# Optimization experiments

Measured on AMD Instinct MI355X. Metric: run time of the kernel, lower is better.

The kernel has to match this reference:

```python
import jax, jax.numpy as jnp
import numpy as np

B, L, D = 4, 8192, 256          # batch, seq length, embedding dim
H, HD = 8, 32                   # heads, head dim (H*HD == D)
WN, P, S = 9, 4, 1              # window size, padding, stride
EPS = 1e-5


def _layer_norm(x, g, b):
    m = jnp.mean(x, axis=-1, keepdims=True)
    v = jnp.mean(jnp.square(x - m), axis=-1, keepdims=True)
    return (x - m) / jnp.sqrt(v + EPS) * g + b


def setup_inputs() -> dict:
    key = jax.random.key(0)
    ks = jax.random.split(key, 8)
    sc = 0.05
    return {
        "x": jax.random.normal(ks[0], (B, L, D), jnp.float32),
        "W_q": jax.random.normal(ks[1], (D, D), jnp.float32) * sc,
        "W_k": jax.random.normal(ks[2], (D, D), jnp.float32) * sc,
        "W_v": jax.random.normal(ks[3], (D, D), jnp.float32) * sc,
        "W_o": jax.random.normal(ks[4], (D, D), jnp.float32) * sc,
        "pos": jax.random.normal(ks[5], (WN, D), jnp.float32) * sc,
        "W_out": jax.random.normal(ks[6], (D, D), jnp.float32) * sc,
        "b_out": jnp.zeros((D,), jnp.float32),
        "g1": jnp.ones((D,), jnp.float32),
        "b1": jnp.zeros((D,), jnp.float32),
        "g2": jnp.ones((D,), jnp.float32),
        "b2": jnp.zeros((D,), jnp.float32),
    }


def reference(x, W_q, W_k, W_v, W_o, pos, W_out, b_out, g1, b1, g2, b2):
    # input_dim == embedding_dim -> no input projection
    padded = jnp.pad(x, ((0, 0), (P, P), (0, 0)))
    nw = (L + 2 * P - WN) // S + 1  # == L for S=1, WN=2P+1
    idx = jnp.arange(nw)[:, None] * S + jnp.arange(WN)[None, :]  # [nw, WN]
    win = padded[:, idx] + pos  # [B, nw, WN, D]

    def proj(w):  # [B, nw, WN, H, HD]
        return jnp.einsum('bnwd,de->bnwe', win, w).reshape(B, nw, WN, H, HD)

    q, k, v = proj(W_q), proj(W_k), proj(W_v)
    scale = 1.0 / (HD ** 0.5)
    scores = jnp.einsum('bnqhd,bnkhd->bnhqk', q, k) * scale  # [B,nw,H,WN,WN]
    attn = jax.nn.softmax(scores, axis=-1)
    # context, summed over query positions within each window (use_mean=False)
    ctx = jnp.einsum('bnhqk,bnkhd->bnhd', attn, v).reshape(B, nw, D)
    skip = x[:, ::S]  # [B, nw, D]
    attn_res = _layer_norm(skip + ctx @ W_o, g1, b1)
    out = _layer_norm(attn_res @ W_out.T + b_out + attn_res, g2, b2)
    return jax.nn.relu(out)
```

## Files before the change

kernel.cpp:

```cpp
#include <hip/hip_runtime.h>
#include <hip/hip_bf16.h>
#include <math.h>

constexpr int NB   = 4;
constexpr int LL   = 8192;
constexpr int DD   = 256;
constexpr int NH   = 8;
constexpr int HDIM = 32;
constexpr int WNN  = 9;
constexpr int PPAD = 4;

constexpr int CW  = 32;
constexpr int RSN = CW + 8;
constexpr int SST = 260;

typedef __attribute__((ext_vector_type(8))) short bf16x8;
typedef __attribute__((ext_vector_type(4))) float f32x4;

__device__ inline short f2bf(float f) {
  __hip_bfloat16 h = __float2bfloat16(f);
  short s; __builtin_memcpy(&s, &h, 2); return s;
}
__device__ inline float bf2f(short s) {
  unsigned u = ((unsigned)(unsigned short)s) << 16;
  float f; __builtin_memcpy(&f, &u, 4); return f;
}

__global__ __launch_bounds__(256) void prep_all(
    const float* __restrict__ Wq, const float* __restrict__ Wk, const float* __restrict__ Wv,
    const float* __restrict__ Wo, const float* __restrict__ Wout, const float* __restrict__ pos,
    short* __restrict__ WqT, short* __restrict__ WkT, short* __restrict__ WvT,
    short* __restrict__ WoT, short* __restrict__ WoutB,
    short* __restrict__ PQb, short* __restrict__ PKb, short* __restrict__ PVb) {
  __shared__ float sm[64 * 65];
  const int t = threadIdx.x, b = blockIdx.x;
  if (b < 64) {
    const int wi = b >> 4, tile = b & 15;
    const int r0 = (tile >> 2) * 64, c0 = (tile & 3) * 64;
    const float* W = (wi == 0) ? Wq : (wi == 1) ? Wk : (wi == 2) ? Wv : Wo;
    short* T = (wi == 0) ? WqT : (wi == 1) ? WkT : (wi == 2) ? WvT : WoT;
    const int tr = t >> 6, tc = t & 63;
#pragma unroll
    for (int i = 0; i < 16; ++i) {
      int r = tr + i * 4;
      sm[r * 65 + tc] = W[(size_t)(r0 + r) * 256 + c0 + tc];
    }
    __syncthreads();
#pragma unroll
    for (int i = 0; i < 16; ++i) {
      int cj = tr + i * 4;
      T[(size_t)(c0 + cj) * 256 + r0 + tc] = f2bf(sm[tc * 65 + cj]);
    }
  } else if (b < 68) {
    const int idx = b - 64;
    for (int i = t; i < 4096; i += 256) {
      float4 v = *(const float4*)(Wout + ((size_t)idx * 4096 + i) * 4);
      short4 o; o.x = f2bf(v.x); o.y = f2bf(v.y); o.z = f2bf(v.z); o.w = f2bf(v.w);
      *(short4*)(WoutB + ((size_t)idx * 4096 + i) * 4) = o;
    }
  } else {
    const int wh = b - 68;
    const float* W = (wh == 0) ? Wq : (wh == 1) ? Wk : Wv;
    short* P = (wh == 0) ? PQb : (wh == 1) ? PKb : PVb;
    for (int i = t; i < WNN * 256; i += 256) sm[i] = pos[i];
    __syncthreads();
    float a[WNN];
#pragma unroll
    for (int w = 0; w < WNN; ++w) a[w] = 0.f;
    for (int d = 0; d < 256; ++d) {
      float wv = W[(size_t)d * 256 + t];
#pragma unroll
      for (int w = 0; w < WNN; ++w) a[w] += sm[w * 256 + d] * wv;
    }
#pragma unroll
    for (int w = 0; w < WNN; ++w) P[w * 256 + t] = f2bf(a[w]);
  }
}

__global__ __launch_bounds__(256) void qkv_fused(
    const float* __restrict__ x,
    const short* __restrict__ WT0, const short* __restrict__ WT1, const short* __restrict__ WT2,
    short* __restrict__ O0, short* __restrict__ O1, short* __restrict__ O2) {
  __shared__ short xs[32 * 264];
  const int t = threadIdx.x, w = t >> 6, lane = t & 63, q = lane >> 4, m = lane & 15;
  const size_t row0 = (size_t)blockIdx.x * 32;

#pragma unroll
  for (int i = 0; i < 8; ++i) {
    int idx = t + i * 256;
    int r = idx >> 6, c4 = (idx & 63) * 4;
    float4 v = *(const float4*)(x + (row0 + r) * 256 + c4);
    short4 o; o.x = f2bf(v.x); o.y = f2bf(v.y); o.z = f2bf(v.z); o.w = f2bf(v.w);
    *(short4*)&xs[r * 264 + c4] = o;
  }
  __syncthreads();

  f32x4 acc[3][2][4];
#pragma unroll
  for (int bu = 0; bu < 3; ++bu)
#pragma unroll
    for (int i = 0; i < 2; ++i)
#pragma unroll
      for (int j = 0; j < 4; ++j) acc[bu][i][j] = (f32x4){0.f, 0.f, 0.f, 0.f};

#pragma unroll
  for (int kk = 0; kk < 8; ++kk) {
    bf16x8 a[2];
#pragma unroll
    for (int i = 0; i < 2; ++i) a[i] = *(const bf16x8*)&xs[(i * 16 + m) * 264 + kk * 32 + q * 8];
#pragma unroll
    for (int bu = 0; bu < 3; ++bu) {
      const short* WT = (bu == 0) ? WT0 : (bu == 1) ? WT1 : WT2;
#pragma unroll
      for (int j = 0; j < 4; ++j) {
        bf16x8 bb = *(const bf16x8*)(WT + (size_t)(w * 64 + j * 16 + m) * 256 + kk * 32 + q * 8);
#pragma unroll
        for (int i = 0; i < 2; ++i)
          acc[bu][i][j] = __builtin_amdgcn_mfma_f32_16x16x32_bf16(a[i], bb, acc[bu][i][j], 0, 0, 0);
      }
    }
  }
#pragma unroll
  for (int bu = 0; bu < 3; ++bu) {
    short* O = (bu == 0) ? O0 : (bu == 1) ? O1 : O2;
#pragma unroll
    for (int i = 0; i < 2; ++i)
#pragma unroll
      for (int j = 0; j < 4; ++j)
#pragma unroll
        for (int r = 0; r < 4; ++r)
          O[(row0 + i * 16 + q * 4 + r) * 256 + w * 64 + j * 16 + m] = f2bf(acc[bu][i][j][r]);
  }
}

__global__ __launch_bounds__(256, 2) void attn_kernel(
    const short* __restrict__ XQb, const short* __restrict__ XKb, const short* __restrict__ XVb,
    const short* __restrict__ PQb, const short* __restrict__ PKb, const short* __restrict__ PVb,
    short* __restrict__ CTXB) {
  __shared__ short sq[RSN * SST];
  __shared__ short sk[RSN * SST];
  __shared__ short sv[RSN * SST];
  __shared__ short pq[WNN * SST];
  __shared__ short pk[WNN * SST];
  __shared__ short pv[WNN * SST];

  const int t = threadIdx.x;
  const int nblk = LL / CW;
  const int b = blockIdx.x / nblk;
  const int n0 = (blockIdx.x % nblk) * CW;
  const size_t base = (size_t)b * LL * DD;

#pragma unroll
  for (int i = 0; i < RSN * 64 / 256; ++i) {
    int idx = t + i * 256;
    int r = idx >> 6, c4 = (idx & 63) * 4;
    int j = n0 - PPAD + r;
    short4 vq = {0, 0, 0, 0}, vk = vq, vv = vq;
    if (j >= 0 && j < LL) {
      size_t off = base + (size_t)j * DD + c4;
      vq = *(const short4*)(XQb + off);
      vk = *(const short4*)(XKb + off);
      vv = *(const short4*)(XVb + off);
    }
    *(short4*)&sq[r * SST + c4] = vq;
    *(short4*)&sk[r * SST + c4] = vk;
    *(short4*)&sv[r * SST + c4] = vv;
  }
#pragma unroll
  for (int i = 0; i < 3; ++i) {
    int idx = t + i * 256;
    if (idx < WNN * 64) {
      int r = idx >> 6, c4 = (idx & 63) * 4;
      *(short4*)&pq[r * SST + c4] = *(const short4*)(PQb + r * DD + c4);
      *(short4*)&pk[r * SST + c4] = *(const short4*)(PKb + r * DD + c4);
      *(short4*)&pv[r * SST + c4] = *(const short4*)(PVb + r * DD + c4);
    }
  }
  __syncthreads();

  const int n = t >> 3;
  const int h = t & 7;
  const int hoff = h * HDIM;

  float sc[WNN][WNN];
#pragma unroll
  for (int qi = 0; qi < WNN; ++qi)
#pragma unroll
    for (int ki = 0; ki < WNN; ++ki) sc[qi][ki] = 0.f;

#pragma unroll
  for (int c = 0; c < 8; ++c) {
    float qv[WNN][4], kv[WNN][4];
#pragma unroll
    for (int r = 0; r < WNN; ++r) {
      short4 xa = *(const short4*)&sq[(n + r) * SST + hoff + c * 4];
      short4 pa = *(const short4*)&pq[r * SST + hoff + c * 4];
      qv[r][0] = bf2f(xa.x) + bf2f(pa.x);
      qv[r][1] = bf2f(xa.y) + bf2f(pa.y);
      qv[r][2] = bf2f(xa.z) + bf2f(pa.z);
      qv[r][3] = bf2f(xa.w) + bf2f(pa.w);
      short4 xb = *(const short4*)&sk[(n + r) * SST + hoff + c * 4];
      short4 pb = *(const short4*)&pk[r * SST + hoff + c * 4];
      kv[r][0] = bf2f(xb.x) + bf2f(pb.x);
      kv[r][1] = bf2f(xb.y) + bf2f(pb.y);
      kv[r][2] = bf2f(xb.z) + bf2f(pb.z);
      kv[r][3] = bf2f(xb.w) + bf2f(pb.w);
    }
#pragma unroll
    for (int qi = 0; qi < WNN; ++qi)
#pragma unroll
      for (int ki = 0; ki < WNN; ++ki)
        sc[qi][ki] += qv[qi][0] * kv[ki][0] + qv[qi][1] * kv[ki][1] +
                      qv[qi][2] * kv[ki][2] + qv[qi][3] * kv[ki][3];
  }

  float cs[WNN];
#pragma unroll
  for (int ki = 0; ki < WNN; ++ki) cs[ki] = 0.f;
  const float scale = 0.17677669529663687f;
#pragma unroll
  for (int qi = 0; qi < WNN; ++qi) {
    float mx = sc[qi][0];
#pragma unroll
    for (int ki = 1; ki < WNN; ++ki) mx = fmaxf(mx, sc[qi][ki]);
    float sum = 0.f;
    float e[WNN];
#pragma unroll
    for (int ki = 0; ki < WNN; ++ki) { e[ki] = __expf((sc[qi][ki] - mx) * scale); sum += e[ki]; }
    float inv = 1.f / sum;
#pragma unroll
    for (int ki = 0; ki < WNN; ++ki) cs[ki] += e[ki] * inv;
  }

#pragma unroll
  for (int c = 0; c < 8; ++c) {
    float o0 = 0.f, o1 = 0.f, o2 = 0.f, o3 = 0.f;
#pragma unroll
    for (int ki = 0; ki < WNN; ++ki) {
      short4 xv4 = *(const short4*)&sv[(n + ki) * SST + hoff + c * 4];
      short4 pv4 = *(const short4*)&pv[ki * SST + hoff + c * 4];
      float wt = cs[ki];
      o0 += wt * (bf2f(xv4.x) + bf2f(pv4.x));
      o1 += wt * (bf2f(xv4.y) + bf2f(pv4.y));
      o2 += wt * (bf2f(xv4.z) + bf2f(pv4.z));
      o3 += wt * (bf2f(xv4.w) + bf2f(pv4.w));
    }
    short4 os; os.x = f2bf(o0); os.y = f2bf(o1); os.z = f2bf(o2); os.w = f2bf(o3);
    *(short4*)(CTXB + base + (size_t)(n0 + n) * DD + hoff + c * 4) = os;
  }
}

__global__ __launch_bounds__(256) void out_mfma(
    const short* __restrict__ CTXB, const float* __restrict__ X,
    const short* __restrict__ WoT, const short* __restrict__ WoutB,
    const float* __restrict__ bo,
    const float* __restrict__ g1, const float* __restrict__ b1,
    const float* __restrict__ g2, const float* __restrict__ b2,
    float* __restrict__ out) {
  __shared__ short ar[64 * 264];
  __shared__ float ws1[64][4], ws2[64][4];
  __shared__ float msh[64], rsh[64];
  __shared__ float g1s[256], b1s[256], g2s[256], b2s[256], bos[256];
  const int t = threadIdx.x, w = t >> 6, lane = t & 63, q = lane >> 4, m = lane & 15;
  const size_t row0 = (size_t)blockIdx.x * 64;
  g1s[t] = g1[t]; b1s[t] = b1[t]; g2s[t] = g2[t]; b2s[t] = b2[t]; bos[t] = bo[t];

  f32x4 acc[4][4];
#pragma unroll
  for (int i = 0; i < 4; ++i)
#pragma unroll
    for (int j = 0; j < 4; ++j) acc[i][j] = (f32x4){0.f, 0.f, 0.f, 0.f};

  const short* abase = CTXB + (row0 + m) * (size_t)256 + q * 8;
  const short* bbase = WoT + (size_t)(w * 64 + m) * 256 + q * 8;
  {
    bf16x8 a[4], b[4];
#pragma unroll
    for (int i = 0; i < 4; ++i) a[i] = *(const bf16x8*)(abase + (size_t)i * 4096);
#pragma unroll
    for (int j = 0; j < 4; ++j) b[j] = *(const bf16x8*)(bbase + (size_t)j * 4096);
#pragma unroll
    for (int kk = 0; kk < 8; ++kk) {
      bf16x8 an[4], bn[4];
      if (kk < 7) {
#pragma unroll
        for (int i = 0; i < 4; ++i) an[i] = *(const bf16x8*)(abase + (size_t)i * 4096 + (kk + 1) * 32);
#pragma unroll
        for (int j = 0; j < 4; ++j) bn[j] = *(const bf16x8*)(bbase + (size_t)j * 4096 + (kk + 1) * 32);
      }
#pragma unroll
      for (int i = 0; i < 4; ++i)
#pragma unroll
        for (int j = 0; j < 4; ++j)
          acc[i][j] = __builtin_amdgcn_mfma_f32_16x16x32_bf16(a[i], b[j], acc[i][j], 0, 0, 0);
      if (kk < 7) {
#pragma unroll
        for (int i = 0; i < 4; ++i) a[i] = an[i];
#pragma unroll
        for (int j = 0; j < 4; ++j) b[j] = bn[j];
      }
    }
  }

  float s1v[4][4], s2v[4][4];
#pragma unroll
  for (int i = 0; i < 4; ++i)
#pragma unroll
    for (int r = 0; r < 4; ++r) {
      float a0 = 0.f, b0 = 0.f;
#pragma unroll
      for (int j = 0; j < 4; ++j) {
        float v = acc[i][j][r] + X[(row0 + i * 16 + q * 4 + r) * 256 + w * 64 + j * 16 + m];
        acc[i][j][r] = v; a0 += v; b0 += v * v;
      }
      s1v[i][r] = a0; s2v[i][r] = b0;
    }
#pragma unroll
  for (int i = 0; i < 4; ++i)
#pragma unroll
    for (int r = 0; r < 4; ++r)
#pragma unroll
      for (int msk = 1; msk < 16; msk <<= 1) {
        s1v[i][r] += __shfl_xor(s1v[i][r], msk, 64);
        s2v[i][r] += __shfl_xor(s2v[i][r], msk, 64);
      }
  if (m == 0) {
#pragma unroll
    for (int i = 0; i < 4; ++i)
#pragma unroll
      for (int r = 0; r < 4; ++r) {
        ws1[i * 16 + q * 4 + r][w] = s1v[i][r];
        ws2[i * 16 + q * 4 + r][w] = s2v[i][r];
      }
  }
  __syncthreads();
  if (t < 64) {
    float a0 = 0.f, b0 = 0.f;
#pragma unroll
    for (int ww = 0; ww < 4; ++ww) { a0 += ws1[t][ww]; b0 += ws2[t][ww]; }
    float mean = a0 * (1.f / 256.f);
    float var = b0 * (1.f / 256.f) - mean * mean;
    msh[t] = mean; rsh[t] = rsqrtf(var + 1e-5f);
  }
  __syncthreads();

#pragma unroll
  for (int i = 0; i < 4; ++i)
#pragma unroll
    for (int r = 0; r < 4; ++r) {
      int row = i * 16 + q * 4 + r;
      float mean = msh[row], rst = rsh[row];
#pragma unroll
      for (int j = 0; j < 4; ++j) {
        int col = w * 64 + j * 16 + m;
        float v = (acc[i][j][r] - mean) * rst * g1s[col] + b1s[col];
        ar[row * 264 + col] = f2bf(v);
      }
    }
  __syncthreads();

#pragma unroll
  for (int i = 0; i < 4; ++i)
#pragma unroll
    for (int j = 0; j < 4; ++j) acc[i][j] = (f32x4){0.f, 0.f, 0.f, 0.f};
  const short* b2base = WoutB + (size_t)(w * 64 + m) * 256 + q * 8;
  {
    bf16x8 b[4];
#pragma unroll
    for (int j = 0; j < 4; ++j) b[j] = *(const bf16x8*)(b2base + (size_t)j * 4096);
#pragma unroll
    for (int kk = 0; kk < 8; ++kk) {
      bf16x8 bn[4];
      if (kk < 7) {
#pragma unroll
        for (int j = 0; j < 4; ++j) bn[j] = *(const bf16x8*)(b2base + (size_t)j * 4096 + (kk + 1) * 32);
      }
      bf16x8 a[4];
#pragma unroll
      for (int i = 0; i < 4; ++i) a[i] = *(const bf16x8*)&ar[(i * 16 + m) * 264 + kk * 32 + q * 8];
#pragma unroll
      for (int i = 0; i < 4; ++i)
#pragma unroll
        for (int j = 0; j < 4; ++j)
          acc[i][j] = __builtin_amdgcn_mfma_f32_16x16x32_bf16(a[i], b[j], acc[i][j], 0, 0, 0);
      if (kk < 7) {
#pragma unroll
        for (int j = 0; j < 4; ++j) b[j] = bn[j];
      }
    }
  }

#pragma unroll
  for (int i = 0; i < 4; ++i)
#pragma unroll
    for (int r = 0; r < 4; ++r) {
      int row = i * 16 + q * 4 + r;
      float a0 = 0.f, b0 = 0.f;
#pragma unroll
      for (int j = 0; j < 4; ++j) {
        int col = w * 64 + j * 16 + m;
        float v = acc[i][j][r] + bos[col] + bf2f(ar[row * 264 + col]);
        acc[i][j][r] = v; a0 += v; b0 += v * v;
      }
      s1v[i][r] = a0; s2v[i][r] = b0;
    }
#pragma unroll
  for (int i = 0; i < 4; ++i)
#pragma unroll
    for (int r = 0; r < 4; ++r)
#pragma unroll
      for (int msk = 1; msk < 16; msk <<= 1) {
        s1v[i][r] += __shfl_xor(s1v[i][r], msk, 64);
        s2v[i][r] += __shfl_xor(s2v[i][r], msk, 64);
      }
  if (m == 0) {
#pragma unroll
    for (int i = 0; i < 4; ++i)
#pragma unroll
      for (int r = 0; r < 4; ++r) {
        ws1[i * 16 + q * 4 + r][w] = s1v[i][r];
        ws2[i * 16 + q * 4 + r][w] = s2v[i][r];
      }
  }
  __syncthreads();
  if (t < 64) {
    float a0 = 0.f, b0 = 0.f;
#pragma unroll
    for (int ww = 0; ww < 4; ++ww) { a0 += ws1[t][ww]; b0 += ws2[t][ww]; }
    float mean = a0 * (1.f / 256.f);
    float var = b0 * (1.f / 256.f) - mean * mean;
    msh[t] = mean; rsh[t] = rsqrtf(var + 1e-5f);
  }
  __syncthreads();

#pragma unroll
  for (int i = 0; i < 4; ++i)
#pragma unroll
    for (int r = 0; r < 4; ++r) {
      int row = i * 16 + q * 4 + r;
      float mean = msh[row], rst = rsh[row];
#pragma unroll
      for (int j = 0; j < 4; ++j) {
        int col = w * 64 + j * 16 + m;
        float v = (acc[i][j][r] - mean) * rst * g2s[col] + b2s[col];
        out[(row0 + row) * 256 + col] = fmaxf(v, 0.f);
      }
    }
}

extern "C" void kernel_launch(void* const* d_in, const int* in_sizes, int n_in,
                              void* d_out, int out_size, void* d_ws, size_t ws_size,
                              hipStream_t stream) {
  const float* x    = (const float*)d_in[0];
  const float* Wq   = (const float*)d_in[1];
  const float* Wk   = (const float*)d_in[2];
  const float* Wv   = (const float*)d_in[3];
  const float* Wo   = (const float*)d_in[4];
  const float* pos  = (const float*)d_in[5];
  const float* Wout = (const float*)d_in[6];
  const float* bo   = (const float*)d_in[7];
  const float* g1   = (const float*)d_in[8];
  const float* b1   = (const float*)d_in[9];
  const float* g2   = (const float*)d_in[10];
  const float* b2   = (const float*)d_in[11];
  float* out = (float*)d_out;

  const size_t nel = (size_t)NB * LL * DD;
  char* wsb = (char*)d_ws;
  short* XQb  = (short*)wsb; wsb += nel * 2;
  short* XKb  = (short*)wsb; wsb += nel * 2;
  short* XVb  = (short*)wsb; wsb += nel * 2;
  short* CTXB = (short*)wsb; wsb += nel * 2;
  short* WqT   = (short*)wsb; wsb += 65536 * 2;
  short* WkT   = (short*)wsb; wsb += 65536 * 2;
  short* WvT   = (short*)wsb; wsb += 65536 * 2;
  short* WoT   = (short*)wsb; wsb += 65536 * 2;
  short* WoutB = (short*)wsb; wsb += 65536 * 2;
  short* PQb = (short*)wsb; wsb += WNN * DD * 2;
  short* PKb = (short*)wsb; wsb += WNN * DD * 2;
  short* PVb = (short*)wsb; wsb += WNN * DD * 2;

  prep_all<<<71, 256, 0, stream>>>(Wq, Wk, Wv, Wo, Wout, pos,
                                   WqT, WkT, WvT, WoT, WoutB, PQb, PKb, PVb);
  qkv_fused<<<(unsigned)(NB * LL / 32), 256, 0, stream>>>(x, WqT, WkT, WvT, XQb, XKb, XVb);
  attn_kernel<<<NB * (LL / CW), 256, 0, stream>>>(XQb, XKb, XVb, PQb, PKb, PVb, CTXB);
  out_mfma<<<(unsigned)(NB * LL / 64), 256, 0, stream>>>(CTXB, x, WoT, WoutB, bo, g1, b1, g2, b2, out);
}
```

Baseline: 273.1 us.

## Fuse QKV projection, windowed attention and output MLP into one kernel

Replaces the three kernels (QKV GEMM, attention, output GEMMs with layer norms) with a single kernel per 16-row chunk. The QKV projection is recomputed over the chunk plus halo rows and kept in shared memory, the context is written back to shared memory, and the two output GEMMs run on 16 rows. This removes the global round trips of the bf16 Q/K/V and context buffers. In exchange it recomputes halo rows (24 of 32 tile rows are useful), lowers MFMA tile reuse, uses a large LDS footprint that may limit occupancy, and splits each head across two threads with a shuffle reduction.

```diff
diff --git a/kernel.cpp b/kernel.cpp
--- a/kernel.cpp
+++ b/kernel.cpp
@@ -6,13 +6,12 @@
 constexpr int LL   = 8192;
 constexpr int DD   = 256;
 constexpr int NH   = 8;
-constexpr int HDIM = 32;
 constexpr int WNN  = 9;
-constexpr int PPAD = 4;
-
-constexpr int CW  = 32;
-constexpr int RSN = CW + 8;
-constexpr int SST = 260;
+
+constexpr int CW   = 16;
+constexpr int RSN  = CW + 8;
+constexpr int SST  = 260;
+constexpr int XST  = 264;
 
 typedef __attribute__((ext_vector_type(8))) short bf16x8;
 typedef __attribute__((ext_vector_type(4))) float f32x4;
@@ -77,94 +76,42 @@
   }
 }
 
-__global__ __launch_bounds__(256) void qkv_fused(
+__global__ __launch_bounds__(256) void mega(
     const float* __restrict__ x,
     const short* __restrict__ WT0, const short* __restrict__ WT1, const short* __restrict__ WT2,
-    short* __restrict__ O0, short* __restrict__ O1, short* __restrict__ O2) {
-  __shared__ short xs[32 * 264];
-  const int t = threadIdx.x, w = t >> 6, lane = t & 63, q = lane >> 4, m = lane & 15;
-  const size_t row0 = (size_t)blockIdx.x * 32;
-
-#pragma unroll
-  for (int i = 0; i < 8; ++i) {
-    int idx = t + i * 256;
-    int r = idx >> 6, c4 = (idx & 63) * 4;
-    float4 v = *(const float4*)(x + (row0 + r) * 256 + c4);
-    short4 o; o.x = f2bf(v.x); o.y = f2bf(v.y); o.z = f2bf(v.z); o.w = f2bf(v.w);
-    *(short4*)&xs[r * 264 + c4] = o;
-  }
-  __syncthreads();
-
-  f32x4 acc[3][2][4];
-#pragma unroll
-  for (int bu = 0; bu < 3; ++bu)
-#pragma unroll
-    for (int i = 0; i < 2; ++i)
-#pragma unroll
-      for (int j = 0; j < 4; ++j) acc[bu][i][j] = (f32x4){0.f, 0.f, 0.f, 0.f};
-
-#pragma unroll
-  for (int kk = 0; kk < 8; ++kk) {
-    bf16x8 a[2];
-#pragma unroll
-    for (int i = 0; i < 2; ++i) a[i] = *(const bf16x8*)&xs[(i * 16 + m) * 264 + kk * 32 + q * 8];
-#pragma unroll
-    for (int bu = 0; bu < 3; ++bu) {
-      const short* WT = (bu == 0) ? WT0 : (bu == 1) ? WT1 : WT2;
-#pragma unroll
-      for (int j = 0; j < 4; ++j) {
-        bf16x8 bb = *(const bf16x8*)(WT + (size_t)(w * 64 + j * 16 + m) * 256 + kk * 32 + q * 8);
-#pragma unroll
-        for (int i = 0; i < 2; ++i)
-          acc[bu][i][j] = __builtin_amdgcn_mfma_f32_16x16x32_bf16(a[i], bb, acc[bu][i][j], 0, 0, 0);
-      }
-    }
-  }
-#pragma unroll
-  for (int bu = 0; bu < 3; ++bu) {
-    short* O = (bu == 0) ? O0 : (bu == 1) ? O1 : O2;
-#pragma unroll
-    for (int i = 0; i < 2; ++i)
-#pragma unroll
-      for (int j = 0; j < 4; ++j)
-#pragma unroll
-        for (int r = 0; r < 4; ++r)
-          O[(row0 + i * 16 + q * 4 + r) * 256 + w * 64 + j * 16 + m] = f2bf(acc[bu][i][j][r]);
-  }
-}
-
-__global__ __launch_bounds__(256, 2) void attn_kernel(
-    const short* __restrict__ XQb, const short* __restrict__ XKb, const short* __restrict__ XVb,
+    const short* __restrict__ WoT, const short* __restrict__ WoutB,
     const short* __restrict__ PQb, const short* __restrict__ PKb, const short* __restrict__ PVb,
-    short* __restrict__ CTXB) {
+    const float* __restrict__ bo,
+    const float* __restrict__ g1, const float* __restrict__ b1,
+    const float* __restrict__ g2, const float* __restrict__ b2,
+    float* __restrict__ out) {
+  __shared__ short xs[32 * XST];
   __shared__ short sq[RSN * SST];
   __shared__ short sk[RSN * SST];
   __shared__ short sv[RSN * SST];
   __shared__ short pq[WNN * SST];
   __shared__ short pk[WNN * SST];
   __shared__ short pv[WNN * SST];
-
-  const int t = threadIdx.x;
+  __shared__ float g1s[256], b1s[256], g2s[256], b2s[256], bos[256];
+  __shared__ float ws1[16][4], ws2[16][4], msh[16], rsh[16];
+
+  const int t = threadIdx.x, w = t >> 6, lane = t & 63, q = lane >> 4, m = lane & 15;
   const int nblk = LL / CW;
-  const int b = blockIdx.x / nblk;
+  const int bb = blockIdx.x / nblk;
   const int n0 = (blockIdx.x % nblk) * CW;
-  const size_t base = (size_t)b * LL * DD;
-
-#pragma unroll
-  for (int i = 0; i < RSN * 64 / 256; ++i) {
+  const size_t rowg0 = (size_t)bb * LL + n0;
+
+  g1s[t] = g1[t]; b1s[t] = b1[t]; g2s[t] = g2[t]; b2s[t] = b2[t]; bos[t] = bo[t];
+
+#pragma unroll
+  for (int i = 0; i < 8; ++i) {
     int idx = t + i * 256;
     int r = idx >> 6, c4 = (idx & 63) * 4;
-    int j = n0 - PPAD + r;
-    short4 vq = {0, 0, 0, 0}, vk = vq, vv = vq;
-    if (j >= 0 && j < LL) {
-      size_t off = base + (size_t)j * DD + c4;
-      vq = *(const short4*)(XQb + off);
-      vk = *(const short4*)(XKb + off);
-      vv = *(const short4*)(XVb + off);
-    }
-    *(short4*)&sq[r * SST + c4] = vq;
-    *(short4*)&sk[r * SST + c4] = vk;
-    *(short4*)&sv[r * SST + c4] = vv;
+    int j = n0 - 4 + r;
+    float4 v = {0.f, 0.f, 0.f, 0.f};
+    if (r < RSN && j >= 0 && j < LL) v = *(const float4*)(x + ((size_t)bb * LL + j) * DD + c4);
+    short4 o; o.x = f2bf(v.x); o.y = f2bf(v.y); o.z = f2bf(v.z); o.w = f2bf(v.w);
+    *(short4*)&xs[r * XST + c4] = o;
   }
 #pragma unroll
   for (int i = 0; i < 3; ++i) {
@@ -178,29 +125,68 @@
   }
   __syncthreads();
 
-  const int n = t >> 3;
-  const int h = t & 7;
-  const int hoff = h * HDIM;
-
+  {
+    f32x4 acc[3][2][4];
+#pragma unroll
+    for (int bu = 0; bu < 3; ++bu)
+#pragma unroll
+      for (int i = 0; i < 2; ++i)
+#pragma unroll
+        for (int j = 0; j < 4; ++j) acc[bu][i][j] = (f32x4){0.f, 0.f, 0.f, 0.f};
+#pragma unroll
+    for (int kk = 0; kk < 8; ++kk) {
+      bf16x8 a[2];
+#pragma unroll
+      for (int i = 0; i < 2; ++i) a[i] = *(const bf16x8*)&xs[(i * 16 + m) * XST + kk * 32 + q * 8];
+#pragma unroll
+      for (int bu = 0; bu < 3; ++bu) {
+        const short* WT = (bu == 0) ? WT0 : (bu == 1) ? WT1 : WT2;
+#pragma unroll
+        for (int j = 0; j < 4; ++j) {
+          bf16x8 bbf = *(const bf16x8*)(WT + (size_t)(w * 64 + j * 16 + m) * 256 + kk * 32 + q * 8);
+#pragma unroll
+          for (int i = 0; i < 2; ++i)
+            acc[bu][i][j] = __builtin_amdgcn_mfma_f32_16x16x32_bf16(a[i], bbf, acc[bu][i][j], 0, 0, 0);
+        }
+      }
+    }
+#pragma unroll
+    for (int bu = 0; bu < 3; ++bu) {
+      short* S = (bu == 0) ? sq : (bu == 1) ? sk : sv;
+#pragma unroll
+      for (int i = 0; i < 2; ++i)
+#pragma unroll
+        for (int j = 0; j < 4; ++j)
+#pragma unroll
+          for (int r = 0; r < 4; ++r) {
+            int rl = i * 16 + q * 4 + r;
+            if (rl < RSN) S[rl * SST + w * 64 + j * 16 + m] = f2bf(acc[bu][i][j][r]);
+          }
+    }
+  }
+  __syncthreads();
+
+  const int n = t >> 4, h = (t >> 1) & 7, half = t & 1;
+  const int so = h * 32 + half * 16;
   float sc[WNN][WNN];
 #pragma unroll
   for (int qi = 0; qi < WNN; ++qi)
 #pragma unroll
     for (int ki = 0; ki < WNN; ++ki) sc[qi][ki] = 0.f;
-
-#pragma unroll
-  for (int c = 0; c < 8; ++c) {
+#pragma unroll
+  for (int c = 0; c < 4; ++c) {
+    const int off = so + c * 4;
     float qv[WNN][4], kv[WNN][4];
 #pragma unroll
     for (int r = 0; r < WNN; ++r) {
-      short4 xa = *(const short4*)&sq[(n + r) * SST + hoff + c * 4];
-      short4 pa = *(const short4*)&pq[r * SST + hoff + c * 4];
+      short4 xa = *(const short4*)&sq[(n + r) * SST + off];
+      short4 pa = *(const short4*)&pq[r * SST + off];
       qv[r][0] = bf2f(xa.x) + bf2f(pa.x);
       qv[r][1] = bf2f(xa.y) + bf2f(pa.y);
       qv[r][2] = bf2f(xa.z) + bf2f(pa.z);
       qv[r][3] = bf2f(xa.w) + bf2f(pa.w);
-      short4 xb = *(const short4*)&sk[(n + r) * SST + hoff + c * 4];
-      short4 pb = *(const short4*)&pk[r * SST + hoff + c * 4];
+      short4 xb = *(const short4*)&sk[(n + r) * SST + off];
+      short4 pb = *(const short4*)&pk[r * SST + off];
       kv[r][0] = bf2f(xb.x) + bf2f(pb.x);
       kv[r][1] = bf2f(xb.y) + bf2f(pb.y);
       kv[r][2] = bf2f(xb.z) + bf2f(pb.z);
@@ -213,6 +199,11 @@
         sc[qi][ki] += qv[qi][0] * kv[ki][0] + qv[qi][1] * kv[ki][1] +
                       qv[qi][2] * kv[ki][2] + qv[qi][3] * kv[ki][3];
   }
+#pragma unroll
+  for (int qi = 0; qi < WNN; ++qi)
+#pragma unroll
+    for (int ki = 0; ki < WNN; ++ki)
+      sc[qi][ki] += __shfl_xor(sc[qi][ki], 1, 64);
 
   float cs[WNN];
 #pragma unroll
@@ -223,8 +214,7 @@
     float mx = sc[qi][0];
 #pragma unroll
     for (int ki = 1; ki < WNN; ++ki) mx = fmaxf(mx, sc[qi][ki]);
-    float sum = 0.f;
-    float e[WNN];
+    float e[WNN], sum = 0.f;
 #pragma unroll
     for (int ki = 0; ki < WNN; ++ki) { e[ki] = __expf((sc[qi][ki] - mx) * scale); sum += e[ki]; }
     float inv = 1.f / sum;
@@ -233,12 +223,13 @@
   }
 
 #pragma unroll
-  for (int c = 0; c < 8; ++c) {
+  for (int c = 0; c < 4; ++c) {
+    const int off = so + c * 4;
     float o0 = 0.f, o1 = 0.f, o2 = 0.f, o3 = 0.f;
 #pragma unroll
     for (int ki = 0; ki < WNN; ++ki) {
-      short4 xv4 = *(const short4*)&sv[(n + ki) * SST + hoff + c * 4];
-      short4 pv4 = *(const short4*)&pv[ki * SST + hoff + c * 4];
+      short4 xv4 = *(const short4*)&sv[(n + ki) * SST + off];
+      short4 pv4 = *(const short4*)&pv[ki * SST + off];
       float wt = cs[ki];
       o0 += wt * (bf2f(xv4.x) + bf2f(pv4.x));
       o1 += wt * (bf2f(xv4.y) + bf2f(pv4.y));
@@ -246,206 +237,126 @@
       o3 += wt * (bf2f(xv4.w) + bf2f(pv4.w));
     }
     short4 os; os.x = f2bf(o0); os.y = f2bf(o1); os.z = f2bf(o2); os.w = f2bf(o3);
-    *(short4*)(CTXB + base + (size_t)(n0 + n) * DD + hoff + c * 4) = os;
-  }
-}
-
-__global__ __launch_bounds__(256) void out_mfma(
-    const short* __restrict__ CTXB, const float* __restrict__ X,
-    const short* __restrict__ WoT, const short* __restrict__ WoutB,
-    const float* __restrict__ bo,
-    const float* __restrict__ g1, const float* __restrict__ b1,
-    const float* __restrict__ g2, const float* __restrict__ b2,
-    float* __restrict__ out) {
-  __shared__ short ar[64 * 264];
-  __shared__ float ws1[64][4], ws2[64][4];
-  __shared__ float msh[64], rsh[64];
-  __shared__ float g1s[256], b1s[256], g2s[256], b2s[256], bos[256];
-  const int t = threadIdx.x, w = t >> 6, lane = t & 63, q = lane >> 4, m = lane & 15;
-  const size_t row0 = (size_t)blockIdx.x * 64;
-  g1s[t] = g1[t]; b1s[t] = b1[t]; g2s[t] = g2[t]; b2s[t] = b2[t]; bos[t] = bo[t];
-
-  f32x4 acc[4][4];
-#pragma unroll
-  for (int i = 0; i < 4; ++i)
-#pragma unroll
-    for (int j = 0; j < 4; ++j) acc[i][j] = (f32x4){0.f, 0.f, 0.f, 0.f};
-
-  const short* abase = CTXB + (row0 + m) * (size_t)256 + q * 8;
-  const short* bbase = WoT + (size_t)(w * 64 + m) * 256 + q * 8;
+    *(short4*)&xs[n * XST + off] = os;
+  }
+  __syncthreads();
+
   {
-    bf16x8 a[4], b[4];
-#pragma unroll
-    for (int i = 0; i < 4; ++i) a[i] = *(const bf16x8*)(abase + (size_t)i * 4096);
-#pragma unroll
-    for (int j = 0; j < 4; ++j) b[j] = *(const bf16x8*)(bbase + (size_t)j * 4096);
+    f32x4 acc1[4];
+#pragma unroll
+    for (int j = 0; j < 4; ++j) acc1[j] = (f32x4){0.f, 0.f, 0.f, 0.f};
 #pragma unroll
     for (int kk = 0; kk < 8; ++kk) {
-      bf16x8 an[4], bn[4];
-      if (kk < 7) {
-#pragma unroll
-        for (int i = 0; i < 4; ++i) an[i] = *(const bf16x8*)(abase + (size_t)i * 4096 + (kk + 1) * 32);
-#pragma unroll
-        for (int j = 0; j < 4; ++j) bn[j] = *(const bf16x8*)(bbase + (size_t)j * 4096 + (kk + 1) * 32);
-      }
-#pragma unroll
-      for (int i = 0; i < 4; ++i)
-#pragma unroll
-        for (int j = 0; j < 4; ++j)
-          acc[i][j] = __builtin_amdgcn_mfma_f32_16x16x32_bf16(a[i], b[j], acc[i][j], 0, 0, 0);
-      if (kk < 7) {
-#pragma unroll
-        for (int i = 0; i < 4; ++i) a[i] = an[i];
-#pragma unroll
-        for (int j = 0; j < 4; ++j) b[j] = bn[j];
-      }
-    }
-  }
-
-  float s1v[4][4], s2v[4][4];
-#pragma unroll
-  for (int i = 0; i < 4; ++i)
+      bf16x8 a = *(const bf16x8*)&xs[m * XST + kk * 32 + q * 8];
+#pragma unroll
+      for (int j = 0; j < 4; ++j) {
+        bf16x8 bbf = *(const bf16x8*)(WoT + (size_t)(w * 64 + j * 16 + m) * 256 + kk * 32 + q * 8);
+        acc1[j] = __builtin_amdgcn_mfma_f32_16x16x32_bf16(a, bbf, acc1[j], 0, 0, 0);
+      }
+    }
+    float s1[4], s2[4];
 #pragma unroll
     for (int r = 0; r < 4; ++r) {
       float a0 = 0.f, b0 = 0.f;
 #pragma unroll
       for (int j = 0; j < 4; ++j) {
-        float v = acc[i][j][r] + X[(row0 + i * 16 + q * 4 + r) * 256 + w * 64 + j * 16 + m];
-        acc[i][j][r] = v; a0 += v; b0 += v * v;
-      }
-      s1v[i][r] = a0; s2v[i][r] = b0;
-    }
-#pragma unroll
-  for (int i = 0; i < 4; ++i)
+        int col = w * 64 + j * 16 + m;
+        float v = acc1[j][r] + x[(rowg0 + q * 4 + r) * 256 + col];
+        acc1[j][r] = v; a0 += v; b0 += v * v;
+      }
+      s1[r] = a0; s2[r] = b0;
+    }
 #pragma unroll
     for (int r = 0; r < 4; ++r)
 #pragma unroll
       for (int msk = 1; msk < 16; msk <<= 1) {
-        s1v[i][r] += __shfl_xor(s1v[i][r], msk, 64);
-        s2v[i][r] += __shfl_xor(s2v[i][r], msk, 64);
-      }
-  if (m == 0) {
-#pragma unroll
-    for (int i = 0; i < 4; ++i)
-#pragma unroll
-      for (int r = 0; r < 4; ++r) {
-        ws1[i * 16 + q * 4 + r][w] = s1v[i][r];
-        ws2[i * 16 + q * 4 + r][w] = s2v[i][r];
-      }
-  }
-  __syncthreads();
-  if (t < 64) {
-    float a0 = 0.f, b0 = 0.f;
-#pragma unroll
-    for (int ww = 0; ww < 4; ++ww) { a0 += ws1[t][ww]; b0 += ws2[t][ww]; }
-    float mean = a0 * (1.f / 256.f);
-    float var = b0 * (1.f / 256.f) - mean * mean;
-    msh[t] = mean; rsh[t] = rsqrtf(var + 1e-5f);
-  }
-  __syncthreads();
-
-#pragma unroll
-  for (int i = 0; i < 4; ++i)
+        s1[r] += __shfl_xor(s1[r], msk, 64);
+        s2[r] += __shfl_xor(s2[r], msk, 64);
+      }
+    if (m == 0) {
+#pragma unroll
+      for (int r = 0; r < 4; ++r) { ws1[q * 4 + r][w] = s1[r]; ws2[q * 4 + r][w] = s2[r]; }
+    }
+    __syncthreads();
+    if (t < 16) {
+      float a0 = 0.f, b0 = 0.f;
+#pragma unroll
+      for (int ww = 0; ww < 4; ++ww) { a0 += ws1[t][ww]; b0 += ws2[t][ww]; }
+      float mean = a0 * (1.f / 256.f);
+      float var = b0 * (1.f / 256.f) - mean * mean;
+      msh[t] = mean; rsh[t] = rsqrtf(var + 1e-5f);
+    }
+    __syncthreads();
 #pragma unroll
     for (int r = 0; r < 4; ++r) {
-      int row = i * 16 + q * 4 + r;
-      float mean = msh[row], rst = rsh[row];
+      int R = q * 4 + r;
+      float mean = msh[R], rst = rsh[R];
 #pragma unroll
       for (int j = 0; j < 4; ++j) {
         int col = w * 64 + j * 16 + m;
-        float v = (acc[i][j][r] - mean) * rst * g1s[col] + b1s[col];
-        ar[row * 264 + col] = f2bf(v);
-      }
-    }
-  __syncthreads();
-
-#pragma unroll
-  for (int i = 0; i < 4; ++i)
-#pragma unroll
-    for (int j = 0; j < 4; ++j) acc[i][j] = (f32x4){0.f, 0.f, 0.f, 0.f};
-  const short* b2base = WoutB + (size_t)(w * 64 + m) * 256 + q * 8;
-  {
-    bf16x8 b[4];
-#pragma unroll
-    for (int j = 0; j < 4; ++j) b[j] = *(const bf16x8*)(b2base + (size_t)j * 4096);
+        float v = (acc1[j][r] - mean) * rst * g1s[col] + b1s[col];
+        xs[(16 + R) * XST + col] = f2bf(v);
+      }
+    }
+    __syncthreads();
+
+    f32x4 acc2[4];
+#pragma unroll
+    for (int j = 0; j < 4; ++j) acc2[j] = (f32x4){0.f, 0.f, 0.f, 0.f};
 #pragma unroll
     for (int kk = 0; kk < 8; ++kk) {
-      bf16x8 bn[4];
-      if (kk < 7) {
-#pragma unroll
-        for (int j = 0; j < 4; ++j) bn[j] = *(const bf16x8*)(b2base + (size_t)j * 4096 + (kk + 1) * 32);
-      }
-      bf16x8 a[4];
-#pragma unroll
-      for (int i = 0; i < 4; ++i) a[i] = *(const bf16x8*)&ar[(i * 16 + m) * 264 + kk * 32 + q * 8];
-#pragma unroll
-      for (int i = 0; i < 4; ++i)
-#pragma unroll
-        for (int j = 0; j < 4; ++j)
-          acc[i][j] = __builtin_amdgcn_mfma_f32_16x16x32_bf16(a[i], b[j], acc[i][j], 0, 0, 0);
-      if (kk < 7) {
-#pragma unroll
-        for (int j = 0; j < 4; ++j) b[j] = bn[j];
-      }
-    }
-  }
-
-#pragma unroll
-  for (int i = 0; i < 4; ++i)
+      bf16x8 a = *(const bf16x8*)&xs[(16 + m) * XST + kk * 32 + q * 8];
+#pragma unroll
+      for (int j = 0; j < 4; ++j) {
+        bf16x8 bbf = *(const bf16x8*)(WoutB + (size_t)(w * 64 + j * 16 + m) * 256 + kk * 32 + q * 8);
+        acc2[j] = __builtin_amdgcn_mfma_f32_16x16x32_bf16(a, bbf, acc2[j], 0, 0, 0);
+      }
+    }
 #pragma unroll
     for (int r = 0; r < 4; ++r) {
-      int row = i * 16 + q * 4 + r;
+      int R = q * 4 + r;
       float a0 = 0.f, b0 = 0.f;
 #pragma unroll
       for (int j = 0; j < 4; ++j) {
         int col = w * 64 + j * 16 + m;
-        float v = acc[i][j][r] + bos[col] + bf2f(ar[row * 264 + col]);
-        acc[i][j][r] = v; a0 += v; b0 += v * v;
-      }
-      s1v[i][r] = a0; s2v[i][r] = b0;
-    }
-#pragma unroll
-  for (int i = 0; i < 4; ++i)
+        float v = acc2[j][r] + bos[col] + bf2f(xs[(16 + R) * XST + col]);
+        acc2[j][r] = v; a0 += v; b0 += v * v;
+      }
+      s1[r] = a0; s2[r] = b0;
+    }
 #pragma unroll
     for (int r = 0; r < 4; ++r)
 #pragma unroll
       for (int msk = 1; msk < 16; msk <<= 1) {
-        s1v[i][r] += __shfl_xor(s1v[i][r], msk, 64);
-        s2v[i][r] += __shfl_xor(s2v[i][r], msk, 64);
-      }
-  if (m == 0) {
-#pragma unroll
-    for (int i = 0; i < 4; ++i)
-#pragma unroll
-      for (int r = 0; r < 4; ++r) {
-        ws1[i * 16 + q * 4 + r][w] = s1v[i][r];
-        ws2[i * 16 + q * 4 + r][w] = s2v[i][r];
-      }
-  }
-  __syncthreads();
-  if (t < 64) {
-    float a0 = 0.f, b0 = 0.f;
-#pragma unroll
-    for (int ww = 0; ww < 4; ++ww) { a0 += ws1[t][ww]; b0 += ws2[t][ww]; }
-    float mean = a0 * (1.f / 256.f);
-    float var = b0 * (1.f / 256.f) - mean * mean;
-    msh[t] = mean; rsh[t] = rsqrtf(var + 1e-5f);
-  }
-  __syncthreads();
-
-#pragma unroll
-  for (int i = 0; i < 4; ++i)
+        s1[r] += __shfl_xor(s1[r], msk, 64);
+        s2[r] += __shfl_xor(s2[r], msk, 64);
+      }
+    if (m == 0) {
+#pragma unroll
+      for (int r = 0; r < 4; ++r) { ws1[q * 4 + r][w] = s1[r]; ws2[q * 4 + r][w] = s2[r]; }
+    }
+    __syncthreads();
+    if (t < 16) {
+      float a0 = 0.f, b0 = 0.f;
+#pragma unroll
+      for (int ww = 0; ww < 4; ++ww) { a0 += ws1[t][ww]; b0 += ws2[t][ww]; }
+      float mean = a0 * (1.f / 256.f);
+      float var = b0 * (1.f / 256.f) - mean * mean;
+      msh[t] = mean; rsh[t] = rsqrtf(var + 1e-5f);
+    }
+    __syncthreads();
 #pragma unroll
     for (int r = 0; r < 4; ++r) {
-      int row = i * 16 + q * 4 + r;
-      float mean = msh[row], rst = rsh[row];
+      int R = q * 4 + r;
+      float mean = msh[R], rst = rsh[R];
 #pragma unroll
       for (int j = 0; j < 4; ++j) {
         int col = w * 64 + j * 16 + m;
-        float v = (acc[i][j][r] - mean) * rst * g2s[col] + b2s[col];
-        out[(row0 + row) * 256 + col] = fmaxf(v, 0.f);
-      }
-    }
+        float v = (acc2[j][r] - mean) * rst * g2s[col] + b2s[col];
+        out[(rowg0 + R) * 256 + col] = fmaxf(v, 0.f);
+      }
+    }
+  }
 }
 
 extern "C" void kernel_launch(void* const* d_in, const int* in_sizes, int n_in,
@@ -465,12 +376,7 @@
   const float* b2   = (const float*)d_in[11];
   float* out = (float*)d_out;
 
-  const size_t nel = (size_t)NB * LL * DD;
   char* wsb = (char*)d_ws;
-  short* XQb  = (short*)wsb; wsb += nel * 2;
-  short* XKb  = (short*)wsb; wsb += nel * 2;
-  short* XVb  = (short*)wsb; wsb += nel * 2;
-  short* CTXB = (short*)wsb; wsb += nel * 2;
   short* WqT   = (short*)wsb; wsb += 65536 * 2;
   short* WkT   = (short*)wsb; wsb += 65536 * 2;
   short* WvT   = (short*)wsb; wsb += 65536 * 2;
@@ -482,7 +388,6 @@
 
   prep_all<<<71, 256, 0, stream>>>(Wq, Wk, Wv, Wo, Wout, pos,
                                    WqT, WkT, WvT, WoT, WoutB, PQb, PKb, PVb);
-  qkv_fused<<<(unsigned)(NB * LL / 32), 256, 0, stream>>>(x, WqT, WkT, WvT, XQb, XKb, XVb);
-  attn_kernel<<<NB * (LL / CW), 256, 0, stream>>>(XQb, XKb, XVb, PQb, PKb, PVb, CTXB);
-  out_mfma<<<(unsigned)(NB * LL / 64), 256, 0, stream>>>(CTXB, x, WoT, WoutB, bo, g1, b1, g2, b2, out);
-}
+  mega<<<NB * (LL / CW), 256, 0, stream>>>(x, WqT, WkT, WvT, WoT, WoutB,
+                                           PQb, PKb, PVb, bo, g1, b1, g2, b2, out);
+}
```

Result: slower. 409.1 us (+49.8%).
